# Kernel tuning notes

Hardware: AMD Instinct MI355X
Metric: run time of the kernel (lower is better)

## Reference

```python
import jax, jax.numpy as jnp
import numpy as np

N_NODES = 50000
N_EDGES = 500000
HIDDEN = 128
HEADS = 8
HEAD_DIM = HIDDEN // HEADS


def setup_inputs() -> dict:
    key = jax.random.key(0)
    ks = jax.random.split(key, 20)

    def lin_w(k, fin, fout):
        return (jax.random.normal(k, (fin, fout), jnp.float32) / np.sqrt(fin)).astype(jnp.float32)

    inp = {
        "h": jax.random.normal(ks[0], (N_NODES, HIDDEN), jnp.float32),
        "x": jax.random.normal(ks[1], (N_NODES, 3), jnp.float32),
        "src": jax.random.randint(ks[2], (N_EDGES,), 0, N_NODES, jnp.int32),
        "dst": jax.random.randint(ks[3], (N_EDGES,), 0, N_NODES, jnp.int32),
        "distances": jax.random.uniform(ks[4], (N_EDGES,), jnp.float32),
        # linear layers stored as [in, out] (transposed vs torch nn.Linear)
        "Wq": lin_w(ks[5], HIDDEN, HIDDEN), "bq": jnp.zeros((HIDDEN,), jnp.float32),
        "Wk": lin_w(ks[6], HIDDEN, HIDDEN), "bk": jnp.zeros((HIDDEN,), jnp.float32),
        "Wv": lin_w(ks[7], HIDDEN, HIDDEN), "bv": jnp.zeros((HIDDEN,), jnp.float32),
        "Wo": lin_w(ks[8], HIDDEN, HIDDEN), "bo": jnp.zeros((HIDDEN,), jnp.float32),
        "Wd": lin_w(ks[9], 1, HEADS), "bd": jnp.zeros((HEADS,), jnp.float32),
        "Wg1": lin_w(ks[10], HIDDEN, HIDDEN), "bg1": jnp.zeros((HIDDEN,), jnp.float32),
        "Wg2": lin_w(ks[11], HIDDEN, 1), "bg2": jnp.zeros((1,), jnp.float32),
    }
    return inp


def reference(h, x, src, dst, distances,
              Wq, bq, Wk, bk, Wv, bv, Wo, bo, Wd, bd, Wg1, bg1, Wg2, bg2):
    n = h.shape[0]
    heads = Wd.shape[1]
    dh = Wq.shape[1] // heads

    q = (h @ Wq + bq).reshape(n, heads, dh)
    k = (h @ Wk + bk).reshape(n, heads, dh)
    v = (h @ Wv + bv).reshape(n, heads, dh)

    q_src = q[src]            # [E, heads, dh]
    k_dst = k[dst]
    v_dst = v[dst]

    logits = jnp.einsum('ehd,ehd->eh', q_src, k_dst) / jnp.sqrt(jnp.asarray(dh, h.dtype))
    bias = (distances * distances)[:, None] @ Wd + bd      # [E, heads]
    lg = logits - bias

    # segment softmax over edges grouped by src node
    m = jax.ops.segment_max(lg, src, num_segments=n)        # [N, heads]
    ex = jnp.exp(lg - m[src])
    s = jax.ops.segment_sum(ex, src, num_segments=n)
    w = ex / jnp.maximum(s[src], 1e-9)                      # [E, heads]

    h_upd = jax.ops.segment_sum(v_dst * w[:, :, None], src, num_segments=n)
    h_out = h + h_upd.reshape(n, heads * dh) @ Wo + bo

    w_mean = w.mean(axis=1)                                 # mean over heads -> [E]
    disp = jax.ops.segment_sum((x[dst] - x[src]) * w_mean[:, None], src, num_segments=n)

    gate = jnp.tanh(jax.nn.silu(h_out @ Wg1 + bg1) @ Wg2 + bg2)  # [N, 1]
    x_out = x + gate * disp
    return (h_out, x_out)
```

## Files before the change

### kernel.cpp

```cpp
#include <hip/hip_runtime.h>
#include <math.h>

#define N_NODES 50000
#define N_EDGES 500000
#define HIDDEN 128
#define HEADS 8
#define HEAD_DIM 16

#define QB 391
#define QKV_TOTAL 782
#define SCAT_BLOCKS 1954
#define SPLITW_BLOCKS 320
#define ZERO_BLOCKS 196

typedef __attribute__((ext_vector_type(8))) short short8;
typedef __attribute__((ext_vector_type(4))) float floatx4;

#define OFF_Q       0u
#define OFF_KV      6400000u
#define OFF_HHI     12800000u
#define OFF_HLO     16000000u
#define OFF_DISP    19200000u
#define OFF_CNT     19350016u
#define OFF_ROWPTR  19400032u
#define OFF_CURSOR  19450048u
#define OFF_ESD     19500064u
#define OFF_WSPLIT  20500064u

static __device__ __forceinline__ unsigned short f2bf(float f) {
    unsigned u = __builtin_bit_cast(unsigned, f);
    unsigned r = (u + 0x7FFFu + ((u >> 16) & 1u)) >> 16;
    return (unsigned short)r;
}
static __device__ __forceinline__ float bf2f(unsigned short s) {
    return __builtin_bit_cast(float, (unsigned)s << 16);
}

__global__ void k_prep(const float* __restrict__ Wq, const float* __restrict__ Wk,
                       const float* __restrict__ Wv, const float* __restrict__ Wo,
                       const float* __restrict__ Wg1, unsigned short* __restrict__ ws,
                       int* __restrict__ cnt) {
    if (blockIdx.x >= SPLITW_BLOCKS) {
        int i = (int)(blockIdx.x - SPLITW_BLOCKS) * 256 + threadIdx.x;
        if (i < N_NODES) cnt[i] = 0;
        return;
    }
    int t = blockIdx.x * 256 + threadIdx.x;
    int m = t >> 14, r = t & 16383;
    int k = r >> 7, n = r & 127;
    const float* W = (m == 0) ? Wq : (m == 1) ? Wk : (m == 2) ? Wv : (m == 3) ? Wo : Wg1;
    float x = W[k * 128 + n];
    int kc = k >> 5, kin = k & 31, quad = kin >> 3, j = kin & 7;
    int ct = n >> 4, nin = n & 15, lane = quad * 16 + nin;
    unsigned base = ((((unsigned)(m * 4 + kc) * 8 + ct) * 2) * 64 + lane) * 8 + j;
    unsigned short a = f2bf(x);
    ws[base] = a;
    ws[base + 512] = f2bf(x - bf2f(a));
}

__global__ void k_count(const int* __restrict__ src, int* __restrict__ cnt,
                        int* __restrict__ rnk) {
    int e = blockIdx.x * 256 + threadIdx.x;
    if (e < N_EDGES) rnk[e] = atomicAdd(&cnt[src[e]], 1);
}

__global__ __launch_bounds__(1024) void k_scan1(const int* __restrict__ cnt,
                                                int* __restrict__ loc,
                                                int* __restrict__ bsum, int n) {
    __shared__ int buf[1024];
    int t = threadIdx.x;
    int i = blockIdx.x * 1024 + t;
    int val = (i < n) ? cnt[i] : 0;
    buf[t] = val;
    __syncthreads();
    for (int off = 1; off < 1024; off <<= 1) {
        int a = (t >= off) ? buf[t - off] : 0;
        __syncthreads();
        buf[t] += a;
        __syncthreads();
    }
    if (i < n) loc[i] = buf[t];
    if (t == 1023) bsum[blockIdx.x] = buf[1023];
}

__global__ __launch_bounds__(256) void k_scan23(const int* __restrict__ loc,
                                                const int* __restrict__ bsum,
                                                int* __restrict__ rowptr, int n, int nb) {
    __shared__ int sb[64];
    int t = threadIdx.x;
    if (t < 64) {
        int v = (t < nb) ? bsum[t] : 0;
        for (int off = 1; off < 64; off <<= 1) {
            int a = __shfl_up(v, off);
            if (t >= off) v += a;
        }
        sb[t] = v;
    }
    __syncthreads();
    int i = blockIdx.x * 256 + t;
    if (i < n) {
        int off = (i >= 1024) ? sb[(i >> 10) - 1] : 0;
        rowptr[i + 1] = loc[i] + off;
    }
    if (i == 0) rowptr[0] = 0;
}

__global__ __launch_bounds__(256) void k_scatter(
    const int* __restrict__ src, const int* __restrict__ dst,
    const float* __restrict__ dist, const int* __restrict__ rowptr,
    const int* __restrict__ rnk, int2* __restrict__ esd) {
    int e = blockIdx.x * 256 + threadIdx.x;
    if (e < N_EDGES) {
        int s = src[e];
        float dd = dist[e];
        int pos = rowptr[s] + rnk[e];
        esd[pos] = make_int2(dst[e], __float_as_int(dd * dd));
    }
}

__global__ __launch_bounds__(256, 2) void k_qkv(
    const float* __restrict__ h, const unsigned short* __restrict__ wsp,
    const float* __restrict__ bq, const float* __restrict__ bk, const float* __restrict__ bv,
    float* __restrict__ q, unsigned* __restrict__ kvp) {
    __shared__ short lds[32768];
    const int tid = threadIdx.x;
    const int wave = tid >> 6, lane = tid & 63;
    const int quad = lane >> 4, l15 = lane & 15;
    const bool iskv = (blockIdx.x >= QB);
    const int blk = iskv ? (int)blockIdx.x - QB : (int)blockIdx.x;
    const int row0 = blk * 128 + wave * 32;

    short8 ah[2][4], al[2][4];
#pragma unroll
    for (int rt = 0; rt < 2; ++rt) {
        int row = row0 + rt * 16 + l15;
        if (row >= N_NODES) row = N_NODES - 1;
        const float* hp = h + (size_t)row * 128;
#pragma unroll
        for (int kc = 0; kc < 4; ++kc) {
            const float* p = hp + kc * 32 + quad * 8;
            float4 f0 = *(const float4*)(p);
            float4 f1 = *(const float4*)(p + 4);
            float fv[8] = {f0.x, f0.y, f0.z, f0.w, f1.x, f1.y, f1.z, f1.w};
#pragma unroll
            for (int j = 0; j < 8; ++j) {
                unsigned short hi = f2bf(fv[j]);
                ah[rt][kc][j] = (short)hi;
                al[rt][kc][j] = (short)f2bf(fv[j] - bf2f(hi));
            }
        }
    }

    auto stage = [&](int m) {
        const float4* s4 = (const float4*)(wsp + (unsigned)m * 32768u);
        float4* d4 = (float4*)lds;
#pragma unroll 4
        for (int it = tid; it < 4096; it += 256) d4[it] = s4[it];
    };

    auto compute = [&](floatx4 (&acc)[2][8]) {
#pragma unroll
        for (int kc = 0; kc < 4; ++kc) {
#pragma unroll
            for (int ct = 0; ct < 8; ++ct) {
                const short* tb = lds + (((kc * 8 + ct) * 2) * 64 + lane) * 8;
                short8 bh = *(const short8*)(tb);
                short8 bl = *(const short8*)(tb + 512);
#pragma unroll
                for (int rt = 0; rt < 2; ++rt) {
                    acc[rt][ct] = __builtin_amdgcn_mfma_f32_16x16x32_bf16(
                        ah[rt][kc], bh, acc[rt][ct], 0, 0, 0);
                    acc[rt][ct] = __builtin_amdgcn_mfma_f32_16x16x32_bf16(
                        ah[rt][kc], bl, acc[rt][ct], 0, 0, 0);
                    acc[rt][ct] = __builtin_amdgcn_mfma_f32_16x16x32_bf16(
                        al[rt][kc], bh, acc[rt][ct], 0, 0, 0);
                }
            }
        }
    };

    if (!iskv) {
        stage(0);
        __syncthreads();
        floatx4 acc[2][8];
#pragma unroll
        for (int rt = 0; rt < 2; ++rt)
#pragma unroll
            for (int ct = 0; ct < 8; ++ct) acc[rt][ct] = (floatx4){0.f, 0.f, 0.f, 0.f};
        compute(acc);
#pragma unroll
        for (int ct = 0; ct < 8; ++ct) {
            int col = ct * 16 + l15;
            float b = bq[col];
#pragma unroll
            for (int rt = 0; rt < 2; ++rt)
#pragma unroll
                for (int reg = 0; reg < 4; ++reg) {
                    int row = row0 + rt * 16 + quad * 4 + reg;
                    if (row < N_NODES) q[(size_t)row * 128 + col] = acc[rt][ct][reg] + b;
                }
        }
    } else {
        stage(1);
        __syncthreads();
        floatx4 acc[2][8];
#pragma unroll
        for (int rt = 0; rt < 2; ++rt)
#pragma unroll
            for (int ct = 0; ct < 8; ++ct) acc[rt][ct] = (floatx4){0.f, 0.f, 0.f, 0.f};
        compute(acc);
        unsigned kb[2][8][2];
#pragma unroll
        for (int ct = 0; ct < 8; ++ct) {
            float b = bk[ct * 16 + l15];
#pragma unroll
            for (int rt = 0; rt < 2; ++rt) {
                kb[rt][ct][0] = (unsigned)f2bf(acc[rt][ct][0] + b) |
                                ((unsigned)f2bf(acc[rt][ct][1] + b) << 16);
                kb[rt][ct][1] = (unsigned)f2bf(acc[rt][ct][2] + b) |
                                ((unsigned)f2bf(acc[rt][ct][3] + b) << 16);
            }
        }
        __syncthreads();
        stage(2);
        __syncthreads();
#pragma unroll
        for (int rt = 0; rt < 2; ++rt)
#pragma unroll
            for (int ct = 0; ct < 8; ++ct) acc[rt][ct] = (floatx4){0.f, 0.f, 0.f, 0.f};
        compute(acc);
#pragma unroll
        for (int ct = 0; ct < 8; ++ct) {
            int col = ct * 16 + l15;
            float b = bv[col];
#pragma unroll
            for (int rt = 0; rt < 2; ++rt)
#pragma unroll
                for (int reg = 0; reg < 4; ++reg) {
                    int row = row0 + rt * 16 + quad * 4 + reg;
                    unsigned vb = f2bf(acc[rt][ct][reg] + b);
                    unsigned kw = (kb[rt][ct][reg >> 1] >> ((reg & 1) * 16)) & 0xFFFFu;
                    if (row < N_NODES) kvp[(size_t)row * 128 + col] = kw | (vb << 16);
                }
        }
    }
}

__global__ __launch_bounds__(256) void k_edge_node(
    const float* __restrict__ q, const unsigned* __restrict__ kvp,
    const float* __restrict__ x,
    const int2* __restrict__ esd, const int* __restrict__ rowptr,
    const float* __restrict__ Wd, const float* __restrict__ bd,
    unsigned short* __restrict__ hupd_hi, unsigned short* __restrict__ hupd_lo,
    float* __restrict__ disp) {
    const int wave = threadIdx.x >> 6, lane = threadIdx.x & 63;
    const int node = blockIdx.x * 4 + wave;
    const int h = lane >> 3, sub = lane & 7;
    const int beg = rowptr[node], end = rowptr[node + 1];

    const float2 qv = *(const float2*)(q + (size_t)node * 128 + 2 * lane);
    const float wdh = Wd[h], bdh = bd[h];
    const bool dal = (sub < 3);
    float xs = dal ? x[node * 3 + sub] : 0.f;
    const unsigned colo = 2 * lane;

    float acc0 = 0.f, acc1 = 0.f, s_own = 0.f, da = 0.f;

    for (int cb = beg; cb < end; cb += 64) {
        int idx = cb + lane;
        int dvec = 0; float d2vec = 0.f;
        if (idx < end) {
            int2 ed = esd[idx];
            dvec = ed.x;
            d2vec = __int_as_float(ed.y);
        }
        int clen = min(64, end - cb);
        int i = 0;
        for (; i + 4 <= clen; i += 4) {
            int di[4]; float dd2[4]; uint2 kv2[4]; float xg[4];
#pragma unroll
            for (int j = 0; j < 4; ++j) {
                di[j]  = __shfl(dvec, i + j);
                dd2[j] = __shfl(d2vec, i + j);
            }
#pragma unroll
            for (int j = 0; j < 4; ++j)
                kv2[j] = *(const uint2*)(kvp + (unsigned)di[j] * 128u + colo);
#pragma unroll
            for (int j = 0; j < 4; ++j)
                xg[j] = dal ? x[(unsigned)di[j] * 3u + sub] : 0.f;
#pragma unroll
            for (int j = 0; j < 4; ++j) {
                float k0 = __builtin_bit_cast(float, kv2[j].x << 16);
                float v0 = __builtin_bit_cast(float, kv2[j].x & 0xFFFF0000u);
                float k1 = __builtin_bit_cast(float, kv2[j].y << 16);
                float v1 = __builtin_bit_cast(float, kv2[j].y & 0xFFFF0000u);
                float p = qv.x * k0 + qv.y * k1;
                p += __shfl_xor(p, 1);
                p += __shfl_xor(p, 2);
                p += __shfl_xor(p, 4);
                float w = __expf(p * 0.25f - (dd2[j] * wdh + bdh));
                s_own += w;
                acc0 += v0 * w;
                acc1 += v1 * w;
                da += (xg[j] - xs) * w;
            }
        }
        for (; i < clen; ++i) {
            int dij  = __shfl(dvec, i);
            float d2 = __shfl(d2vec, i);
            uint2 kv2 = *(const uint2*)(kvp + (unsigned)dij * 128u + colo);
            float xgj = dal ? x[(unsigned)dij * 3u + sub] : 0.f;
            float k0 = __builtin_bit_cast(float, kv2.x << 16);
            float v0 = __builtin_bit_cast(float, kv2.x & 0xFFFF0000u);
            float k1 = __builtin_bit_cast(float, kv2.y << 16);
            float v1 = __builtin_bit_cast(float, kv2.y & 0xFFFF0000u);
            float p = qv.x * k0 + qv.y * k1;
            p += __shfl_xor(p, 1);
            p += __shfl_xor(p, 2);
            p += __shfl_xor(p, 4);
            float w = __expf(p * 0.25f - (d2 * wdh + bdh));
            s_own += w;
            acc0 += v0 * w;
            acc1 += v1 * w;
            da += (xgj - xs) * w;
        }
    }

    float inva = 1.f / fmaxf(s_own, 1e-9f);
    float o0 = acc0 * inva, o1 = acc1 * inva;
    unsigned short h0 = f2bf(o0), h1 = f2bf(o1);
    unsigned short l0 = f2bf(o0 - bf2f(h0)), l1 = f2bf(o1 - bf2f(h1));
    ((unsigned*)hupd_hi)[(size_t)node * 64 + lane] = (unsigned)h0 | ((unsigned)h1 << 16);
    ((unsigned*)hupd_lo)[(size_t)node * 64 + lane] = (unsigned)l0 | ((unsigned)l1 << 16);

    da *= 0.125f * inva;
    da += __shfl_xor(da, 8);
    da += __shfl_xor(da, 16);
    da += __shfl_xor(da, 32);
    if (lane < 3) disp[node * 3 + lane] = da;
}

__global__ __launch_bounds__(256) void k_hout_gate(
    const float* __restrict__ h,
    const unsigned short* __restrict__ hupd_hi, const unsigned short* __restrict__ hupd_lo,
    const unsigned short* __restrict__ wsp,
    const float* __restrict__ bo, const float* __restrict__ bg1,
    const float* __restrict__ Wg2, const float* __restrict__ bg2,
    const float* __restrict__ x, const float* __restrict__ disp,
    float* __restrict__ hout, float* __restrict__ xout) {
    __shared__ float hb[4][16 * 132];
    const int wave = threadIdx.x >> 6, lane = threadIdx.x & 63;
    const int quad = lane >> 4, l15 = lane & 15;
    const int row0 = blockIdx.x * 64 + wave * 16;
    float* hbw = hb[wave];

    floatx4 acc[8];
#pragma unroll
    for (int c = 0; c < 8; ++c) acc[c] = (floatx4){0.f, 0.f, 0.f, 0.f};
#pragma unroll
    for (int kc = 0; kc < 4; ++kc) {
        int row = row0 + l15;
        if (row >= N_NODES) row = N_NODES - 1;
        size_t aoff = (size_t)row * 128 + kc * 32 + quad * 8;
        short8 ah = *(const short8*)(hupd_hi + aoff);
        short8 al = *(const short8*)(hupd_lo + aoff);
#pragma unroll
        for (int ct = 0; ct < 8; ++ct) {
            unsigned fb = ((((unsigned)(3 * 4 + kc) * 8 + ct) * 2) * 64 + lane) * 8;
            short8 bh = *(const short8*)(wsp + fb);
            short8 bl = *(const short8*)(wsp + fb + 512);
            acc[ct] = __builtin_amdgcn_mfma_f32_16x16x32_bf16(ah, bh, acc[ct], 0, 0, 0);
            acc[ct] = __builtin_amdgcn_mfma_f32_16x16x32_bf16(ah, bl, acc[ct], 0, 0, 0);
            acc[ct] = __builtin_amdgcn_mfma_f32_16x16x32_bf16(al, bh, acc[ct], 0, 0, 0);
        }
    }

#pragma unroll
    for (int ct = 0; ct < 8; ++ct) {
        int col = ct * 16 + l15;
        float bias = bo[col];
#pragma unroll
        for (int reg = 0; reg < 4; ++reg) {
            int row = row0 + quad * 4 + reg;
            float val = acc[ct][reg] + bias;
            if (row < N_NODES) {
                val += h[(size_t)row * 128 + col];
                hout[(size_t)row * 128 + col] = val;
            }
            hbw[(quad * 4 + reg) * 132 + col] = val;
        }
    }
    __asm__ volatile("s_waitcnt lgkmcnt(0)" ::: "memory");

    floatx4 acc2[8];
#pragma unroll
    for (int c = 0; c < 8; ++c) acc2[c] = (floatx4){0.f, 0.f, 0.f, 0.f};
#pragma unroll
    for (int kc = 0; kc < 4; ++kc) {
        const float* ap = hbw + l15 * 132 + kc * 32 + quad * 8;
        float4 f0 = *(const float4*)(ap);
        float4 f1 = *(const float4*)(ap + 4);
        float fv[8] = {f0.x, f0.y, f0.z, f0.w, f1.x, f1.y, f1.z, f1.w};
        short8 ah, al;
#pragma unroll
        for (int j = 0; j < 8; ++j) {
            unsigned short hi = f2bf(fv[j]);
            ah[j] = (short)hi;
            al[j] = (short)f2bf(fv[j] - bf2f(hi));
        }
#pragma unroll
        for (int ct = 0; ct < 8; ++ct) {
            unsigned fb = ((((unsigned)(4 * 4 + kc) * 8 + ct) * 2) * 64 + lane) * 8;
            short8 bh = *(const short8*)(wsp + fb);
            short8 bl = *(const short8*)(wsp + fb + 512);
            acc2[ct] = __builtin_amdgcn_mfma_f32_16x16x32_bf16(ah, bh, acc2[ct], 0, 0, 0);
            acc2[ct] = __builtin_amdgcn_mfma_f32_16x16x32_bf16(ah, bl, acc2[ct], 0, 0, 0);
            acc2[ct] = __builtin_amdgcn_mfma_f32_16x16x32_bf16(al, bh, acc2[ct], 0, 0, 0);
        }
    }

    float pr[4] = {0.f, 0.f, 0.f, 0.f};
#pragma unroll
    for (int ct = 0; ct < 8; ++ct) {
        int col = ct * 16 + l15;
        float b1 = bg1[col];
        float w2 = Wg2[col];
#pragma unroll
        for (int reg = 0; reg < 4; ++reg) {
            float z = acc2[ct][reg] + b1;
            pr[reg] += (z / (1.f + __expf(-z))) * w2;
        }
    }
#pragma unroll
    for (int off = 1; off < 16; off <<= 1) {
#pragma unroll
        for (int reg = 0; reg < 4; ++reg) pr[reg] += __shfl_xor(pr[reg], off);
    }
    if (l15 == 0) {
        float b2 = bg2[0];
#pragma unroll
        for (int reg = 0; reg < 4; ++reg) {
            int row = row0 + quad * 4 + reg;
            if (row < N_NODES) {
                float g = tanhf(pr[reg] + b2);
#pragma unroll
                for (int dd = 0; dd < 3; ++dd) {
                    int oo = row * 3 + dd;
                    xout[oo] = x[oo] + g * disp[oo];
                }
            }
        }
    }
}

extern "C" void kernel_launch(void* const* d_in, const int* in_sizes, int n_in,
                              void* d_out, int out_size, void* d_ws, size_t ws_size,
                              hipStream_t stream) {
    const float* h    = (const float*)d_in[0];
    const float* x    = (const float*)d_in[1];
    const int*   src  = (const int*)d_in[2];
    const int*   dst  = (const int*)d_in[3];
    const float* dist = (const float*)d_in[4];
    const float* Wq = (const float*)d_in[5];  const float* bq = (const float*)d_in[6];
    const float* Wk = (const float*)d_in[7];  const float* bk = (const float*)d_in[8];
    const float* Wv = (const float*)d_in[9];  const float* bv = (const float*)d_in[10];
    const float* Wo = (const float*)d_in[11]; const float* bo = (const float*)d_in[12];
    const float* Wd = (const float*)d_in[13]; const float* bd = (const float*)d_in[14];
    const float* Wg1 = (const float*)d_in[15]; const float* bg1 = (const float*)d_in[16];
    const float* Wg2 = (const float*)d_in[17]; const float* bg2 = (const float*)d_in[18];

    float* ws    = (float*)d_ws;
    float* q     = ws + OFF_Q;
    unsigned* kvp = (unsigned*)(ws + OFF_KV);
    float* disp  = ws + OFF_DISP;
    int* cnt     = (int*)(ws + OFF_CNT);
    int* rowptr  = (int*)(ws + OFF_ROWPTR);
    int2* esd    = (int2*)(ws + OFF_ESD);
    unsigned short* wsp = (unsigned short*)(ws + OFF_WSPLIT);
    int* loc    = (int*)(ws + OFF_Q);
    int* bsum   = (int*)(ws + OFF_Q + 500000u);
    int* rank   = (int*)(ws + OFF_HHI);
    unsigned short* hupd_hi = (unsigned short*)(ws + OFF_HHI);
    unsigned short* hupd_lo = (unsigned short*)(ws + OFF_HLO);
    float* hout = (float*)d_out;
    float* xout = hout + (size_t)N_NODES * HIDDEN;

    const int nscan = (N_NODES + 1023) / 1024;

    k_prep<<<SPLITW_BLOCKS + ZERO_BLOCKS, 256, 0, stream>>>(Wq, Wk, Wv, Wo, Wg1, wsp, cnt);
    k_count<<<SCAT_BLOCKS, 256, 0, stream>>>(src, cnt, rank);
    k_scan1<<<nscan, 1024, 0, stream>>>(cnt, loc, bsum, N_NODES);
    k_scan23<<<ZERO_BLOCKS, 256, 0, stream>>>(loc, bsum, rowptr, N_NODES, nscan);
    k_scatter<<<SCAT_BLOCKS, 256, 0, stream>>>(src, dst, dist, rowptr, rank, esd);
    k_qkv<<<QKV_TOTAL, 256, 0, stream>>>(h, wsp, bq, bk, bv, q, kvp);
    k_edge_node<<<N_NODES / 4, 256, 0, stream>>>(q, kvp, x, esd, rowptr,
                                                 Wd, bd, hupd_hi, hupd_lo, disp);
    k_hout_gate<<<(N_NODES + 63) / 64, 256, 0, stream>>>(h, hupd_hi, hupd_lo, wsp,
                                                         bo, bg1, Wg2, bg2,
                                                         x, disp, hout, xout);
}
```

Before: 266.9 us.

## Stage Wo/Wg1 weights in LDS and simplify edge loop with direct edge loads

The edge kernel stops doing a cooperative 64-edge load plus shuffle broadcast. Each lane now loads esd entries directly, which are uniform broadcast loads. It also folds the 1/sqrt(dh) scale into q and drops the bd bias, which cancels in the softmax. The output/gate kernel moves to 512-thread blocks of 128 rows and stages each 64KB weight matrix into LDS once per block, instead of every wave reading the B fragments from global memory. The extra syncthreads and the large LDS footprint may lower occupancy. Dropping bd relies on the shift-invariance of softmax; no row-max is applied in either version.

```diff
diff --git a/kernel.cpp b/kernel.cpp
--- a/kernel.cpp
+++ b/kernel.cpp
@@ -258,73 +258,60 @@
     const int h = lane >> 3, sub = lane & 7;
     const int beg = rowptr[node], end = rowptr[node + 1];
 
-    const float2 qv = *(const float2*)(q + (size_t)node * 128 + 2 * lane);
-    const float wdh = Wd[h], bdh = bd[h];
+    float2 qv = *(const float2*)(q + (size_t)node * 128 + 2 * lane);
+    qv.x *= 0.25f; qv.y *= 0.25f;
+    const float wdh = Wd[h];
     const bool dal = (sub < 3);
     float xs = dal ? x[node * 3 + sub] : 0.f;
     const unsigned colo = 2 * lane;
 
     float acc0 = 0.f, acc1 = 0.f, s_own = 0.f, da = 0.f;
 
-    for (int cb = beg; cb < end; cb += 64) {
-        int idx = cb + lane;
-        int dvec = 0; float d2vec = 0.f;
-        if (idx < end) {
-            int2 ed = esd[idx];
-            dvec = ed.x;
-            d2vec = __int_as_float(ed.y);
-        }
-        int clen = min(64, end - cb);
-        int i = 0;
-        for (; i + 4 <= clen; i += 4) {
-            int di[4]; float dd2[4]; uint2 kv2[4]; float xg[4];
-#pragma unroll
-            for (int j = 0; j < 4; ++j) {
-                di[j]  = __shfl(dvec, i + j);
-                dd2[j] = __shfl(d2vec, i + j);
-            }
-#pragma unroll
-            for (int j = 0; j < 4; ++j)
-                kv2[j] = *(const uint2*)(kvp + (unsigned)di[j] * 128u + colo);
-#pragma unroll
-            for (int j = 0; j < 4; ++j)
-                xg[j] = dal ? x[(unsigned)di[j] * 3u + sub] : 0.f;
-#pragma unroll
-            for (int j = 0; j < 4; ++j) {
-                float k0 = __builtin_bit_cast(float, kv2[j].x << 16);
-                float v0 = __builtin_bit_cast(float, kv2[j].x & 0xFFFF0000u);
-                float k1 = __builtin_bit_cast(float, kv2[j].y << 16);
-                float v1 = __builtin_bit_cast(float, kv2[j].y & 0xFFFF0000u);
-                float p = qv.x * k0 + qv.y * k1;
-                p += __shfl_xor(p, 1);
-                p += __shfl_xor(p, 2);
-                p += __shfl_xor(p, 4);
-                float w = __expf(p * 0.25f - (dd2[j] * wdh + bdh));
-                s_own += w;
-                acc0 += v0 * w;
-                acc1 += v1 * w;
-                da += (xg[j] - xs) * w;
-            }
-        }
-        for (; i < clen; ++i) {
-            int dij  = __shfl(dvec, i);
-            float d2 = __shfl(d2vec, i);
-            uint2 kv2 = *(const uint2*)(kvp + (unsigned)dij * 128u + colo);
-            float xgj = dal ? x[(unsigned)dij * 3u + sub] : 0.f;
-            float k0 = __builtin_bit_cast(float, kv2.x << 16);
-            float v0 = __builtin_bit_cast(float, kv2.x & 0xFFFF0000u);
-            float k1 = __builtin_bit_cast(float, kv2.y << 16);
-            float v1 = __builtin_bit_cast(float, kv2.y & 0xFFFF0000u);
+    int e = beg;
+    for (; e + 4 <= end; e += 4) {
+        int2 ed[4]; uint2 kv2[4]; float xg[4];
+#pragma unroll
+        for (int j = 0; j < 4; ++j) ed[j] = esd[e + j];
+#pragma unroll
+        for (int j = 0; j < 4; ++j)
+            kv2[j] = *(const uint2*)(kvp + (unsigned)ed[j].x * 128u + colo);
+#pragma unroll
+        for (int j = 0; j < 4; ++j)
+            xg[j] = dal ? x[(unsigned)ed[j].x * 3u + sub] : 0.f;
+#pragma unroll
+        for (int j = 0; j < 4; ++j) {
+            float k0 = __builtin_bit_cast(float, kv2[j].x << 16);
+            float v0 = __builtin_bit_cast(float, kv2[j].x & 0xFFFF0000u);
+            float k1 = __builtin_bit_cast(float, kv2[j].y << 16);
+            float v1 = __builtin_bit_cast(float, kv2[j].y & 0xFFFF0000u);
             float p = qv.x * k0 + qv.y * k1;
             p += __shfl_xor(p, 1);
             p += __shfl_xor(p, 2);
             p += __shfl_xor(p, 4);
-            float w = __expf(p * 0.25f - (d2 * wdh + bdh));
+            float w = __expf(p - __int_as_float(ed[j].y) * wdh);
             s_own += w;
             acc0 += v0 * w;
             acc1 += v1 * w;
-            da += (xgj - xs) * w;
-        }
+            da += (xg[j] - xs) * w;
+        }
+    }
+    for (; e < end; ++e) {
+        int2 ed = esd[e];
+        uint2 kv2 = *(const uint2*)(kvp + (unsigned)ed.x * 128u + colo);
+        float xgj = dal ? x[(unsigned)ed.x * 3u + sub] : 0.f;
+        float k0 = __builtin_bit_cast(float, kv2.x << 16);
+        float v0 = __builtin_bit_cast(float, kv2.x & 0xFFFF0000u);
+        float k1 = __builtin_bit_cast(float, kv2.y << 16);
+        float v1 = __builtin_bit_cast(float, kv2.y & 0xFFFF0000u);
+        float p = qv.x * k0 + qv.y * k1;
+        p += __shfl_xor(p, 1);
+        p += __shfl_xor(p, 2);
+        p += __shfl_xor(p, 4);
+        float w = __expf(p - __int_as_float(ed.y) * wdh);
+        s_own += w;
+        acc0 += v0 * w;
+        acc1 += v1 * w;
+        da += (xgj - xs) * w;
     }
 
     float inva = 1.f / fmaxf(s_own, 1e-9f);
@@ -341,7 +328,7 @@
     if (lane < 3) disp[node * 3 + lane] = da;
 }
 
-__global__ __launch_bounds__(256) void k_hout_gate(
+__global__ __launch_bounds__(512) void k_hout_gate(
     const float* __restrict__ h,
     const unsigned short* __restrict__ hupd_hi, const unsigned short* __restrict__ hupd_lo,
     const unsigned short* __restrict__ wsp,
@@ -349,30 +336,50 @@
     const float* __restrict__ Wg2, const float* __restrict__ bg2,
     const float* __restrict__ x, const float* __restrict__ disp,
     float* __restrict__ hout, float* __restrict__ xout) {
-    __shared__ float hb[4][16 * 132];
-    const int wave = threadIdx.x >> 6, lane = threadIdx.x & 63;
+    __shared__ short wlds[32768];
+    __shared__ float hb[8][16 * 132];
+    const int tid = threadIdx.x;
+    const int wave = tid >> 6, lane = tid & 63;
     const int quad = lane >> 4, l15 = lane & 15;
-    const int row0 = blockIdx.x * 64 + wave * 16;
+    const int row0 = blockIdx.x * 128 + wave * 16;
     float* hbw = hb[wave];
 
-    floatx4 acc[8];
-#pragma unroll
-    for (int c = 0; c < 8; ++c) acc[c] = (floatx4){0.f, 0.f, 0.f, 0.f};
-#pragma unroll
-    for (int kc = 0; kc < 4; ++kc) {
+    auto stage = [&](int m) {
+        const float4* s4 = (const float4*)(wsp + (unsigned)m * 32768u);
+        float4* d4 = (float4*)wlds;
+#pragma unroll 2
+        for (int it = tid; it < 4096; it += 512) d4[it] = s4[it];
+    };
+
+    stage(3);
+
+    short8 ah[4], al[4];
+    {
         int row = row0 + l15;
         if (row >= N_NODES) row = N_NODES - 1;
-        size_t aoff = (size_t)row * 128 + kc * 32 + quad * 8;
-        short8 ah = *(const short8*)(hupd_hi + aoff);
-        short8 al = *(const short8*)(hupd_lo + aoff);
+        size_t base = (size_t)row * 128;
+#pragma unroll
+        for (int kc = 0; kc < 4; ++kc) {
+            size_t aoff = base + kc * 32 + quad * 8;
+            ah[kc] = *(const short8*)(hupd_hi + aoff);
+            al[kc] = *(const short8*)(hupd_lo + aoff);
+        }
+    }
+    __syncthreads();
+
+    floatx4 acc[8];
+#pragma unroll
+    for (int c = 0; c < 8; ++c) acc[c] = (floatx4){0.f, 0.f, 0.f, 0.f};
+#pragma unroll
+    for (int kc = 0; kc < 4; ++kc) {
 #pragma unroll
         for (int ct = 0; ct < 8; ++ct) {
-            unsigned fb = ((((unsigned)(3 * 4 + kc) * 8 + ct) * 2) * 64 + lane) * 8;
-            short8 bh = *(const short8*)(wsp + fb);
-            short8 bl = *(const short8*)(wsp + fb + 512);
-            acc[ct] = __builtin_amdgcn_mfma_f32_16x16x32_bf16(ah, bh, acc[ct], 0, 0, 0);
-            acc[ct] = __builtin_amdgcn_mfma_f32_16x16x32_bf16(ah, bl, acc[ct], 0, 0, 0);
-            acc[ct] = __builtin_amdgcn_mfma_f32_16x16x32_bf16(al, bh, acc[ct], 0, 0, 0);
+            const short* tb = wlds + (((kc * 8 + ct) * 2) * 64 + lane) * 8;
+            short8 bh = *(const short8*)(tb);
+            short8 bl = *(const short8*)(tb + 512);
+            acc[ct] = __builtin_amdgcn_mfma_f32_16x16x32_bf16(ah[kc], bh, acc[ct], 0, 0, 0);
+            acc[ct] = __builtin_amdgcn_mfma_f32_16x16x32_bf16(ah[kc], bl, acc[ct], 0, 0, 0);
+            acc[ct] = __builtin_amdgcn_mfma_f32_16x16x32_bf16(al[kc], bh, acc[ct], 0, 0, 0);
         }
     }
 
@@ -391,7 +398,10 @@
             hbw[(quad * 4 + reg) * 132 + col] = val;
         }
     }
-    __asm__ volatile("s_waitcnt lgkmcnt(0)" ::: "memory");
+    __syncthreads();
+
+    stage(4);
+    __syncthreads();
 
     floatx4 acc2[8];
 #pragma unroll
@@ -402,21 +412,21 @@
         float4 f0 = *(const float4*)(ap);
         float4 f1 = *(const float4*)(ap + 4);
         float fv[8] = {f0.x, f0.y, f0.z, f0.w, f1.x, f1.y, f1.z, f1.w};
-        short8 ah, al;
+        short8 a2h, a2l;
 #pragma unroll
         for (int j = 0; j < 8; ++j) {
             unsigned short hi = f2bf(fv[j]);
-            ah[j] = (short)hi;
-            al[j] = (short)f2bf(fv[j] - bf2f(hi));
+            a2h[j] = (short)hi;
+            a2l[j] = (short)f2bf(fv[j] - bf2f(hi));
         }
 #pragma unroll
         for (int ct = 0; ct < 8; ++ct) {
-            unsigned fb = ((((unsigned)(4 * 4 + kc) * 8 + ct) * 2) * 64 + lane) * 8;
-            short8 bh = *(const short8*)(wsp + fb);
-            short8 bl = *(const short8*)(wsp + fb + 512);
-            acc2[ct] = __builtin_amdgcn_mfma_f32_16x16x32_bf16(ah, bh, acc2[ct], 0, 0, 0);
-            acc2[ct] = __builtin_amdgcn_mfma_f32_16x16x32_bf16(ah, bl, acc2[ct], 0, 0, 0);
-            acc2[ct] = __builtin_amdgcn_mfma_f32_16x16x32_bf16(al, bh, acc2[ct], 0, 0, 0);
+            const short* tb = wlds + (((kc * 8 + ct) * 2) * 64 + lane) * 8;
+            short8 bh = *(const short8*)(tb);
+            short8 bl = *(const short8*)(tb + 512);
+            acc2[ct] = __builtin_amdgcn_mfma_f32_16x16x32_bf16(a2h, bh, acc2[ct], 0, 0, 0);
+            acc2[ct] = __builtin_amdgcn_mfma_f32_16x16x32_bf16(a2h, bl, acc2[ct], 0, 0, 0);
+            acc2[ct] = __builtin_amdgcn_mfma_f32_16x16x32_bf16(a2l, bh, acc2[ct], 0, 0, 0);
         }
     }
 
@@ -496,7 +506,7 @@
     k_qkv<<<QKV_TOTAL, 256, 0, stream>>>(h, wsp, bq, bk, bv, q, kvp);
     k_edge_node<<<N_NODES / 4, 256, 0, stream>>>(q, kvp, x, esd, rowptr,
                                                  Wd, bd, hupd_hi, hupd_lo, disp);
-    k_hout_gate<<<(N_NODES + 63) / 64, 256, 0, stream>>>(h, hupd_hi, hupd_lo, wsp,
-                                                         bo, bg1, Wg2, bg2,
-                                                         x, disp, hout, xout);
-}
+    k_hout_gate<<<QB, 512, 0, stream>>>(h, hupd_hi, hupd_lo, wsp,
+                                        bo, bg1, Wg2, bg2,
+                                        x, disp, hout, xout);
+}
```

Result: slower. 279.6 us (+4.7%).
